# Optimization experiments

Measured on AMD Instinct MI355X. Metric: run time of the kernel, lower is better.

## Reference

```python
import jax, jax.numpy as jnp
import numpy as np

B, NAT, K, F, L = 16, 256, 24, 128, 4
EPS = 0.01  # action / displacement step scale


def _gather(a, idx):
    # a: [B, n, ...], idx: [B, n, k] -> [B, n, k, ...]
    return jax.vmap(lambda ab, ib: ab[ib])(a, idx)


def _knn_idx(x, cell, k):
    # periodic minimum-image kNN within each structure
    frac = x[:, None, :, :] - x[:, :, None, :]          # [B,i,j,3] = x_j - x_i
    frac = frac - jnp.round(frac)
    cart = jnp.einsum('bijd,bde->bije', frac, cell)
    dist = jnp.linalg.norm(cart, axis=-1)
    dist = dist + jnp.eye(x.shape[1], dtype=x.dtype) * 1e6  # exclude self
    _, idx = jax.lax.top_k(-dist, k)
    return idx


def _edge_vectors(x, cell, idx):
    xj = _gather(x, idx)                                # [B,n,k,3]
    frac = xj - x[:, :, None, :]
    frac = frac - jnp.round(frac)
    vec = jnp.einsum('bnkd,bde->bnke', frac, cell)
    dist = jnp.linalg.norm(vec, axis=-1)
    return vec, dist


def _mpnn(h, idx, dist, W1, b1, W2, b2):
    hj = _gather(h, idx)                                # [B,n,k,F]
    feat = jnp.concatenate([hj, dist[..., None]], axis=-1)
    m = jax.nn.silu(jnp.einsum('bnkf,fg->bnkg', feat, W1) + b1)
    return h + jax.nn.silu(m.sum(axis=2) @ W2 + b2)


def _forward(cell, x, z, emb, mW1, mb1, mW2, mb2, uW1, ub1, uW2, ub2, act_we, actpos_we):
    I = jnp.eye(3, dtype=x.dtype)
    Bc = cell.shape[0]
    cell0 = jnp.broadcast_to(I, (Bc, 3, 3))            # actions_init overrides input cell
    x = jnp.mod(x, 1.0)
    idx = _knn_idx(x, cell0, K)
    vec, dist = _edge_vectors(x, cell0, idx)
    u = vec / (dist[..., None] + 1e-12)
    cross = jnp.cross(u[:, :, :, None, :], u[:, :, None, :, :])  # [B,n,k,k,3]
    tri_mask = (jnp.linalg.norm(cross, axis=-1) > 1e-3).astype(x.dtype)  # filter_triplets

    h = emb[z]
    for l in range(L):
        h = _mpnn(h, idx, dist, mW1[l], mb1[l], mW2[l], mb2[l])

    action_rho = jnp.broadcast_to(I, (Bc, 3, 3))
    traj_sum = jnp.zeros_like(x)
    geo_cell = cell0
    rho_prime = action_rho
    for l in range(L):
        h = _mpnn(h, idx, dist, uW1[l], ub1[l], uW2[l], ub2[l])
        hj = _gather(h, idx)
        e_feat = h[:, :, None, :] + hj                  # [B,n,k,F]
        w_e = jnp.tanh(jnp.einsum('bnkf,f->bnk', e_feat, act_we[l]))
        w_t = w_e[:, :, :, None] * w_e[:, :, None, :] * tri_mask
        strain = jnp.einsum('bnk,bnkc,bnkd->bcd', w_e, u, u) / (NAT * K)
        tri = jnp.einsum('bnjk,bnjkc,bnjkd->bcd', w_t, cross, cross) / (NAT * K * K)
        action = jnp.eye(3, dtype=x.dtype) + EPS * (strain + tri)
        action_rho = jnp.einsum('bij,bjk->bik', action, action_rho)
        rho_prime = jnp.einsum('bij,bjk->bik', action_rho, cell0)
        # position actions
        w_p = jnp.tanh(jnp.einsum('bnkf,f->bnk', e_feat, actpos_we[l]))
        x_cart = EPS * jnp.einsum('bnk,bnkc->bnc', w_p, vec)
        x_frac = jnp.einsum('bnc,bcd->bnd', x_cart, jnp.linalg.inv(geo_cell))
        traj_sum = traj_sum + x_cart
        x = x + x_frac
        geo_cell = rho_prime
        vec, dist = _edge_vectors(x, geo_cell, idx)     # geometry.update_vectors()
        u = vec / (dist[..., None] + 1e-12)
        cross = jnp.cross(u[:, :, :, None, :], u[:, :, None, :, :])
    return traj_sum, rho_prime


def setup_inputs() -> dict:
    key = jax.random.key(0)
    ks = jax.random.split(key, 12)
    s1 = 1.0 / np.sqrt(F + 1)
    s2 = 1.0 / np.sqrt(F)
    return {
        'cell': jax.random.normal(ks[0], (B, 3, 3), jnp.float32),
        'x': jax.random.uniform(ks[1], (B, NAT, 3), jnp.float32),
        'z': jax.random.randint(ks[2], (B, NAT), 0, 100, dtype=jnp.int32),
        'struct_size': jnp.full((B,), NAT, dtype=jnp.int32),
        'emb': jax.random.normal(ks[3], (100, F), jnp.float32) * 0.1,
        'mpnn_W1': jax.random.normal(ks[4], (L, F + 1, F), jnp.float32) * s1,
        'mpnn_b1': jnp.zeros((L, F), jnp.float32),
        'mpnn_W2': jax.random.normal(ks[5], (L, F, F), jnp.float32) * s2,
        'mpnn_b2': jnp.zeros((L, F), jnp.float32),
        'upd_W1': jax.random.normal(ks[6], (L, F + 1, F), jnp.float32) * s1,
        'upd_b1': jnp.zeros((L, F), jnp.float32),
        'upd_W2': jax.random.normal(ks[7], (L, F, F), jnp.float32) * s2,
        'upd_b2': jnp.zeros((L, F), jnp.float32),
        'act_we': jax.random.normal(ks[8], (L, F), jnp.float32) * s2,
        'actpos_we': jax.random.normal(ks[9], (L, F), jnp.float32) * s2,
    }


def reference(cell, x, z, struct_size, emb, mpnn_W1, mpnn_b1, mpnn_W2, mpnn_b2, upd_W1, upd_b1, upd_W2, upd_b2, act_we, actpos_we):
    # struct_size is informational (dense uniform batch of NAT atoms per structure)
    return _forward(cell, x, z, emb, mpnn_W1, mpnn_b1, mpnn_W2, mpnn_b2,
                    upd_W1, upd_b1, upd_W2, upd_b2, act_we, actpos_we)
```

## Files before the change

kernel.cpp:

```cpp
#include <hip/hip_runtime.h>

#define NB 16
#define NATS 256
#define KNN 24
#define FD 128
#define EPSA 0.01f
#define NATOMS (NB * NATS)
#define NEDGE (NATOMS * KNN)

__device__ __forceinline__ float silu_f(float v) { return v / (1.f + __expf(-v)); }

__global__ __launch_bounds__(256) void init_gemm1_kernel(
    const float* __restrict__ xin, const int* __restrict__ z,
    const float* __restrict__ emb, const float* __restrict__ W1,
    float* __restrict__ x, float* __restrict__ traj,
    float* __restrict__ h, float* __restrict__ hW)
{
    __shared__ float As[128 * 18];
    __shared__ float Bs[128 * 128];
    const int t = threadIdx.x;
    const int atom0 = blockIdx.x * 16;
    if (t < 48) {
        int gi = atom0 * 3 + t;
        float v = xin[gi];
        x[gi] = v - floorf(v);
        traj[gi] = 0.f;
    }
    {
        const int r = t >> 4;
        const int f0 = (t & 15) * 8;
        const int a = atom0 + r;
        const float4* src = (const float4*)(emb + z[a] * FD + f0);
        float4 v0 = src[0], v1 = src[1];
        float4* dst = (float4*)(h + a * FD + f0);
        dst[0] = v0; dst[1] = v1;
        As[(f0 + 0) * 18 + r] = v0.x; As[(f0 + 1) * 18 + r] = v0.y;
        As[(f0 + 2) * 18 + r] = v0.z; As[(f0 + 3) * 18 + r] = v0.w;
        As[(f0 + 4) * 18 + r] = v1.x; As[(f0 + 5) * 18 + r] = v1.y;
        As[(f0 + 6) * 18 + r] = v1.z; As[(f0 + 7) * 18 + r] = v1.w;
    }
    {
        const float4* B4 = (const float4*)W1;
        float4* Bs4 = (float4*)Bs;
#pragma unroll
        for (int i = 0; i < 16; ++i) Bs4[t + i * 256] = B4[t + i * 256];
    }
    __syncthreads();
    const int ng = t & 31, mg = t >> 5;
    const int n0 = ng * 4, m0 = mg * 2;
    float a00 = 0, a01 = 0, a02 = 0, a03 = 0, a10 = 0, a11 = 0, a12 = 0, a13 = 0;
#pragma unroll 8
    for (int f = 0; f < 128; ++f) {
        float2 av = *(const float2*)&As[f * 18 + m0];
        float4 bv = *(const float4*)&Bs[f * FD + n0];
        a00 += av.x * bv.x; a01 += av.x * bv.y; a02 += av.x * bv.z; a03 += av.x * bv.w;
        a10 += av.y * bv.x; a11 += av.y * bv.y; a12 += av.y * bv.z; a13 += av.y * bv.w;
    }
    int row = atom0 + m0;
    *(float4*)(hW + row * FD + n0) = make_float4(a00, a01, a02, a03);
    *(float4*)(hW + (row + 1) * FD + n0) = make_float4(a10, a11, a12, a13);
}

__global__ __launch_bounds__(64) void knn_kernel(const float* __restrict__ x,
    int* __restrict__ idxb, float* __restrict__ u0, float* __restrict__ dist0)
{
    const int a = blockIdx.x;
    const int b = a >> 8;
    const int lane = threadIdx.x;
    const float xi0 = x[a * 3 + 0], xi1 = x[a * 3 + 1], xi2 = x[a * 3 + 2];
    unsigned long long key[4];
#pragma unroll
    for (int tt = 0; tt < 4; ++tt) {
        int jg = b * NATS + lane + tt * 64;
        float d0 = x[jg * 3 + 0] - xi0; d0 -= rintf(d0);
        float d1 = x[jg * 3 + 1] - xi1; d1 -= rintf(d1);
        float d2 = x[jg * 3 + 2] - xi2; d2 -= rintf(d2);
        float dd = sqrtf(d0 * d0 + d1 * d1 + d2 * d2);
        if (jg == a) dd += 1e6f;
        key[tt] = ((unsigned long long)__float_as_uint(dd) << 32) | (unsigned)jg;
    }
    int myj = 0;
    for (int sel = 0; sel < KNN; ++sel) {
        unsigned long long m = key[0];
        if (key[1] < m) m = key[1];
        if (key[2] < m) m = key[2];
        if (key[3] < m) m = key[3];
#pragma unroll
        for (int off = 32; off > 0; off >>= 1) {
            unsigned lo = (unsigned)__shfl_xor((int)(unsigned)(m & 0xffffffffu), off);
            unsigned hi = (unsigned)__shfl_xor((int)(unsigned)(m >> 32), off);
            unsigned long long o = ((unsigned long long)hi << 32) | lo;
            if (o < m) m = o;
        }
        int jw = (int)(m & 0xffffffffu);
        if (lane == 0) idxb[a * KNN + sel] = jw;
        if (lane == sel) myj = jw;
#pragma unroll
        for (int tt = 0; tt < 4; ++tt) if (key[tt] == m) key[tt] = ~0ull;
    }
    if (lane < KNN) {
        float f0 = x[myj * 3 + 0] - xi0; f0 -= rintf(f0);
        float f1 = x[myj * 3 + 1] - xi1; f1 -= rintf(f1);
        float f2 = x[myj * 3 + 2] - xi2; f2 -= rintf(f2);
        float dd = sqrtf(f0 * f0 + f1 * f1 + f2 * f2);
        float inv = 1.f / (dd + 1e-12f);
        int e = a * KNN + lane;
        u0[e * 3 + 0] = f0 * inv; u0[e * 3 + 1] = f1 * inv; u0[e * 3 + 2] = f2 * inv;
        dist0[e] = dd;
    }
}

__global__ __launch_bounds__(256, 2) void layer_kernel(
    const float* __restrict__ hW, const int* __restrict__ idxb,
    const float* __restrict__ dist0,
    const float* __restrict__ x, const float* __restrict__ geo, int use_geo,
    const float* __restrict__ wl, const float* __restrict__ b1,
    const float* __restrict__ W2, const float* __restrict__ b2,
    const float* __restrict__ W1n, float* __restrict__ hWout,
    float* __restrict__ h,
    const float* __restrict__ we_a, const float* __restrict__ we_p,
    float* __restrict__ p, float* __restrict__ q)
{
    __shared__ float As[128 * 9];
    __shared__ float sH[128 * 9];
    __shared__ float Bs[128 * 128];
    __shared__ int   sIdx[8 * KNN];
    __shared__ float sDist[8 * KNN];
    const int t = threadIdx.x;
    const int atom0 = blockIdx.x * 8;
    if (t < 8 * KNN) {
        int a = atom0 + (t / KNN);
        int j = idxb[atom0 * KNN + t];
        sIdx[t] = j;
        float d;
        if (dist0 != nullptr) {
            d = dist0[atom0 * KNN + t];
        } else {
            float f0 = x[j * 3 + 0] - x[a * 3 + 0]; f0 -= rintf(f0);
            float f1 = x[j * 3 + 1] - x[a * 3 + 1]; f1 -= rintf(f1);
            float f2 = x[j * 3 + 2] - x[a * 3 + 2]; f2 -= rintf(f2);
            float v0 = f0, v1 = f1, v2 = f2;
            if (use_geo) {
                const float* c = geo + (a >> 8) * 9;
                v0 = f0 * c[0] + f1 * c[3] + f2 * c[6];
                v1 = f0 * c[1] + f1 * c[4] + f2 * c[7];
                v2 = f0 * c[2] + f1 * c[5] + f2 * c[8];
            }
            d = sqrtf(v0 * v0 + v1 * v1 + v2 * v2);
        }
        sDist[t] = d;
    }
    __syncthreads();
    {
        const int g = t & 127;
        const int sub = t >> 7;
        const float wlg = wl[g];
        const float b1g = b1[g];
#pragma unroll
        for (int rep = 0; rep < 4; ++rep) {
            const int a = rep * 2 + sub;
            float s = 0.f;
#pragma unroll 8
            for (int k = 0; k < KNN; ++k) {
                int j = sIdx[a * KNN + k];
                float v = hW[j * FD + g] + sDist[a * KNN + k] * wlg + b1g;
                s += silu_f(v);
            }
            As[g * 9 + a] = s;
        }
    }
    {
        const float4* B4 = (const float4*)W2;
        float4* Bs4 = (float4*)Bs;
#pragma unroll
        for (int i = 0; i < 16; ++i) Bs4[t + i * 256] = B4[t + i * 256];
    }
    __syncthreads();
    const int ng = t & 31, mg = t >> 5;
    const int n0 = ng * 4;
    float c0 = 0, c1 = 0, c2 = 0, c3 = 0;
#pragma unroll 8
    for (int f = 0; f < 128; ++f) {
        float av = As[f * 9 + mg];
        float4 bv = *(const float4*)&Bs[f * FD + n0];
        c0 += av * bv.x; c1 += av * bv.y; c2 += av * bv.z; c3 += av * bv.w;
    }
    const int row = atom0 + mg;
    float4 bb = *(const float4*)(b2 + n0);
    float4 h0 = *(float4*)(h + row * FD + n0);
    float4 o0;
    o0.x = h0.x + silu_f(c0 + bb.x); o0.y = h0.y + silu_f(c1 + bb.y);
    o0.z = h0.z + silu_f(c2 + bb.z); o0.w = h0.w + silu_f(c3 + bb.w);
    *(float4*)(h + row * FD + n0) = o0;
    sH[(n0 + 0) * 9 + mg] = o0.x; sH[(n0 + 1) * 9 + mg] = o0.y;
    sH[(n0 + 2) * 9 + mg] = o0.z; sH[(n0 + 3) * 9 + mg] = o0.w;
    if (we_a != nullptr) {
        float4 wa = *(const float4*)(we_a + n0);
        float4 wp = *(const float4*)(we_p + n0);
        float p0 = o0.x * wa.x + o0.y * wa.y + o0.z * wa.z + o0.w * wa.w;
        float q0 = o0.x * wp.x + o0.y * wp.y + o0.z * wp.z + o0.w * wp.w;
#pragma unroll
        for (int off = 16; off > 0; off >>= 1) {
            p0 += __shfl_xor(p0, off); q0 += __shfl_xor(q0, off);
        }
        if (ng == 0) { p[row] = p0; q[row] = q0; }
    }
    if (W1n != nullptr) {
        __syncthreads();
        {
            const float4* B4 = (const float4*)W1n;
            float4* Bs4 = (float4*)Bs;
#pragma unroll
            for (int i = 0; i < 16; ++i) Bs4[t + i * 256] = B4[t + i * 256];
        }
        __syncthreads();
        float d0 = 0, d1 = 0, d2 = 0, d3 = 0;
#pragma unroll 8
        for (int f = 0; f < 128; ++f) {
            float av = sH[f * 9 + mg];
            float4 bv = *(const float4*)&Bs[f * FD + n0];
            d0 += av * bv.x; d1 += av * bv.y; d2 += av * bv.z; d3 += av * bv.w;
        }
        *(float4*)(hWout + row * FD + n0) = make_float4(d0, d1, d2, d3);
    }
}

__global__ __launch_bounds__(256) void accum_kernel(
    const float* __restrict__ p, const float* __restrict__ q,
    const int* __restrict__ idxb, const float* __restrict__ x,
    const float* __restrict__ geo, int use_geo,
    const float* __restrict__ u0b,
    float* __restrict__ part, float* __restrict__ xcart)
{
    const int blk = blockIdx.x;
    const int t = threadIdx.x;
    const int w = t >> 6;
    const int lane = t & 63;
    const int a = blk * 4 + w;
    const int b = a >> 8;
    __shared__ float swe[4][KNN], swp[4][KNN];
    __shared__ float su[4][KNN][3], su0[4][KNN][3], sv[4][KNN][3];
    __shared__ float spart[4][18];
    if (lane < KNN) {
        int e = a * KNN + lane;
        int j = idxb[e];
        swe[w][lane] = tanhf(p[a] + p[j]);
        swp[w][lane] = tanhf(q[a] + q[j]);
        float f0 = x[j * 3 + 0] - x[a * 3 + 0]; f0 -= rintf(f0);
        float f1 = x[j * 3 + 1] - x[a * 3 + 1]; f1 -= rintf(f1);
        float f2 = x[j * 3 + 2] - x[a * 3 + 2]; f2 -= rintf(f2);
        float v0 = f0, v1 = f1, v2 = f2;
        if (use_geo) {
            const float* c = geo + b * 9;
            v0 = f0 * c[0] + f1 * c[3] + f2 * c[6];
            v1 = f0 * c[1] + f1 * c[4] + f2 * c[7];
            v2 = f0 * c[2] + f1 * c[5] + f2 * c[8];
        }
        float dd = sqrtf(v0 * v0 + v1 * v1 + v2 * v2);
        float inv = 1.f / (dd + 1e-12f);
        sv[w][lane][0] = v0; sv[w][lane][1] = v1; sv[w][lane][2] = v2;
        su[w][lane][0] = v0 * inv; su[w][lane][1] = v1 * inv; su[w][lane][2] = v2 * inv;
        su0[w][lane][0] = u0b[e * 3]; su0[w][lane][1] = u0b[e * 3 + 1]; su0[w][lane][2] = u0b[e * 3 + 2];
    }
    __syncthreads();
    float r[21];
#pragma unroll
    for (int i = 0; i < 21; ++i) r[i] = 0.f;
    if (lane < KNN) {
        float wgt = swe[w][lane];
        float ux = su[w][lane][0], uy = su[w][lane][1], uz = su[w][lane][2];
        r[0] = wgt * ux * ux; r[1] = wgt * ux * uy; r[2] = wgt * ux * uz;
        r[3] = wgt * uy * ux; r[4] = wgt * uy * uy; r[5] = wgt * uy * uz;
        r[6] = wgt * uz * ux; r[7] = wgt * uz * uy; r[8] = wgt * uz * uz;
        float wp = swp[w][lane];
        r[18] = wp * sv[w][lane][0]; r[19] = wp * sv[w][lane][1]; r[20] = wp * sv[w][lane][2];
    }
#pragma unroll
    for (int tt = 0; tt < 9; ++tt) {
        int pr = lane + (tt << 6);
        int j = pr / KNN, k = pr - j * KNN;
        float c0x = su0[w][j][1] * su0[w][k][2] - su0[w][j][2] * su0[w][k][1];
        float c0y = su0[w][j][2] * su0[w][k][0] - su0[w][j][0] * su0[w][k][2];
        float c0z = su0[w][j][0] * su0[w][k][1] - su0[w][j][1] * su0[w][k][0];
        float nn2 = c0x * c0x + c0y * c0y + c0z * c0z;
        if (nn2 > 1e-6f) {
            float cx = su[w][j][1] * su[w][k][2] - su[w][j][2] * su[w][k][1];
            float cy = su[w][j][2] * su[w][k][0] - su[w][j][0] * su[w][k][2];
            float cz = su[w][j][0] * su[w][k][1] - su[w][j][1] * su[w][k][0];
            float wt = swe[w][j] * swe[w][k];
            r[9]  += wt * cx * cx; r[10] += wt * cx * cy; r[11] += wt * cx * cz;
            r[12] += wt * cy * cx; r[13] += wt * cy * cy; r[14] += wt * cy * cz;
            r[15] += wt * cz * cx; r[16] += wt * cz * cy; r[17] += wt * cz * cz;
        }
    }
#pragma unroll
    for (int off = 32; off > 0; off >>= 1)
#pragma unroll
        for (int i = 0; i < 21; ++i) r[i] += __shfl_down(r[i], off);
    if (lane == 0) {
#pragma unroll
        for (int i = 0; i < 18; ++i) spart[w][i] = r[i];
        xcart[a * 3 + 0] = EPSA * r[18];
        xcart[a * 3 + 1] = EPSA * r[19];
        xcart[a * 3 + 2] = EPSA * r[20];
    }
    __syncthreads();
    if (t < 18)
        part[blk * 18 + t] = spart[0][t] + spart[1][t] + spart[2][t] + spart[3][t];
}

__global__ __launch_bounds__(256) void rho_pos_kernel(const float* __restrict__ part,
    const float* __restrict__ xcart,
    float* __restrict__ rho, float* __restrict__ geo,
    float* __restrict__ x, float* __restrict__ traj,
    float* __restrict__ out, int first, int last)
{
    const int b = blockIdx.x;
    const int t = threadIdx.x;
    __shared__ float sIV[9];
    if (t < 64) {
        float r[18];
#pragma unroll
        for (int i = 0; i < 18; ++i) r[i] = part[(b * 64 + t) * 18 + i];
#pragma unroll
        for (int off = 32; off > 0; off >>= 1)
#pragma unroll
            for (int i = 0; i < 18; ++i) r[i] += __shfl_down(r[i], off);
        if (t == 0) {
            float A[9];
#pragma unroll
            for (int i = 0; i < 9; ++i) {
                float strain = r[i] / 6144.f;
                float tri = r[9 + i] / 147456.f;
                A[i] = ((i == 0 || i == 4 || i == 8) ? 1.f : 0.f) + EPSA * (strain + tri);
            }
            float N[9], IV[9];
            if (first) {
#pragma unroll
                for (int i = 0; i < 9; ++i) { N[i] = A[i]; IV[i] = (i == 0 || i == 4 || i == 8) ? 1.f : 0.f; }
            } else {
                float R[9], G[9];
#pragma unroll
                for (int i = 0; i < 9; ++i) { R[i] = rho[b * 9 + i]; G[i] = geo[b * 9 + i]; }
#pragma unroll
                for (int i = 0; i < 3; ++i)
#pragma unroll
                    for (int k = 0; k < 3; ++k)
                        N[i * 3 + k] = A[i * 3] * R[k] + A[i * 3 + 1] * R[3 + k] + A[i * 3 + 2] * R[6 + k];
                float det = G[0] * (G[4] * G[8] - G[5] * G[7])
                          - G[1] * (G[3] * G[8] - G[5] * G[6])
                          + G[2] * (G[3] * G[7] - G[4] * G[6]);
                float id = 1.f / det;
                IV[0] = (G[4] * G[8] - G[5] * G[7]) * id;
                IV[1] = (G[2] * G[7] - G[1] * G[8]) * id;
                IV[2] = (G[1] * G[5] - G[2] * G[4]) * id;
                IV[3] = (G[5] * G[6] - G[3] * G[8]) * id;
                IV[4] = (G[0] * G[8] - G[2] * G[6]) * id;
                IV[5] = (G[2] * G[3] - G[0] * G[5]) * id;
                IV[6] = (G[3] * G[7] - G[4] * G[6]) * id;
                IV[7] = (G[1] * G[6] - G[0] * G[7]) * id;
                IV[8] = (G[0] * G[4] - G[1] * G[3]) * id;
            }
#pragma unroll
            for (int i = 0; i < 9; ++i) {
                sIV[i] = IV[i];
                rho[b * 9 + i] = N[i];
                if (!last) geo[b * 9 + i] = N[i];
                else out[NATOMS * 3 + b * 9 + i] = N[i];
            }
        }
    }
    __syncthreads();
    for (int d = t; d < NATS * 3; d += 256) {
        int al = d / 3, dim = d - al * 3;
        int ga = b * NATS + al;
        int gi = ga * 3 + dim;
        float c0 = xcart[ga * 3 + 0], c1 = xcart[ga * 3 + 1], c2 = xcart[ga * 3 + 2];
        float tj = traj[gi] + xcart[gi];
        if (!last) {
            float xf = c0 * sIV[0 + dim] + c1 * sIV[3 + dim] + c2 * sIV[6 + dim];
            x[gi] += xf;
            traj[gi] = tj;
        } else {
            out[gi] = tj;
        }
    }
}

extern "C" void kernel_launch(void* const* d_in, const int* in_sizes, int n_in,
                              void* d_out, int out_size, void* d_ws, size_t ws_size,
                              hipStream_t stream)
{
    (void)in_sizes; (void)n_in; (void)out_size; (void)ws_size;
    const float* in_x = (const float*)d_in[1];
    const int*   z    = (const int*)d_in[2];
    const float* emb  = (const float*)d_in[4];
    const float* mW1  = (const float*)d_in[5];
    const float* mb1  = (const float*)d_in[6];
    const float* mW2  = (const float*)d_in[7];
    const float* mb2  = (const float*)d_in[8];
    const float* uW1  = (const float*)d_in[9];
    const float* ub1  = (const float*)d_in[10];
    const float* uW2  = (const float*)d_in[11];
    const float* ub2  = (const float*)d_in[12];
    const float* awe  = (const float*)d_in[13];
    const float* pwe  = (const float*)d_in[14];
    float* out = (float*)d_out;

    char* wsb = (char*)d_ws;
    size_t off = 0;
    auto carve = [&](size_t elems) {
        void* ptr = wsb + off;
        off += (elems * 4 + 255) & ~(size_t)255;
        return ptr;
    };
    float* traj  = (float*)carve(NATOMS * 3);
    float* part  = (float*)carve(1024 * 18);
    float* x     = (float*)carve(NATOMS * 3);
    float* xcart = (float*)carve(NATOMS * 3);
    float* p     = (float*)carve(NATOMS);
    float* q     = (float*)carve(NATOMS);
    float* rho   = (float*)carve(NB * 9);
    float* geo   = (float*)carve(NB * 9);
    float* u0    = (float*)carve(NEDGE * 3);
    float* dist0 = (float*)carve(NEDGE);
    float* h     = (float*)carve(NATOMS * FD);
    float* hWa   = (float*)carve(NATOMS * FD);
    float* hWb   = (float*)carve(NATOMS * FD);
    int*   idx   = (int*)carve(NEDGE);

    init_gemm1_kernel<<<256, 256, 0, stream>>>(in_x, z, emb, mW1, x, traj, h, hWa);
    knn_kernel<<<NATOMS, 64, 0, stream>>>(x, idx, u0, dist0);

    float* hw_in = hWa;
    float* hw_out = hWb;

    for (int l = 0; l < 4; ++l) {
        const float* W1n = (l < 3) ? (mW1 + (l + 1) * 129 * 128) : uW1;
        layer_kernel<<<512, 256, 0, stream>>>(hw_in, idx, dist0, x, geo, 0,
            mW1 + l * 129 * 128 + 128 * 128, mb1 + l * 128,
            mW2 + l * 128 * 128, mb2 + l * 128,
            W1n, hw_out, h,
            nullptr, nullptr, nullptr, nullptr);
        float* tmp = hw_in; hw_in = hw_out; hw_out = tmp;
    }
    for (int l = 0; l < 4; ++l) {
        const float* W1n = (l < 3) ? (uW1 + (l + 1) * 129 * 128) : nullptr;
        const float* d0 = (l == 0) ? dist0 : nullptr;
        layer_kernel<<<512, 256, 0, stream>>>(hw_in, idx, d0, x, geo, (l > 0) ? 1 : 0,
            uW1 + l * 129 * 128 + 128 * 128, ub1 + l * 128,
            uW2 + l * 128 * 128, ub2 + l * 128,
            W1n, hw_out, h,
            awe + l * 128, pwe + l * 128, p, q);
        float* tmp = hw_in; hw_in = hw_out; hw_out = tmp;
        accum_kernel<<<1024, 256, 0, stream>>>(p, q, idx, x, geo, (l > 0) ? 1 : 0,
            u0, part, xcart);
        rho_pos_kernel<<<NB, 256, 0, stream>>>(part, xcart, rho, geo, x, traj, out,
            (l == 0) ? 1 : 0, (l == 3) ? 1 : 0);
    }
}
```

Before: 347.5 us.

## Use split-bf16 MFMA for dense GEMMs with pre-transposed bf16 weight pairs

Adds a prep kernel that transposes every W1/W2 weight matrix and splits it into high and low bf16 halves. The init and layer GEMMs now run on 16x16x32 bf16 MFMA with three products per tile (hi*hi, hi*lo, lo*hi) to keep near-fp32 accuracy. The 64KB fp32 weight staging in LDS is removed in favour of direct global loads of B fragments, which also cuts LDS use per block. Only half of each 16-row MFMA tile holds real atoms in layer_kernel, so half the matrix work is wasted. The h write is also skipped on the last layer, and the geo transform is applied unconditionally.

```diff
diff --git a/kernel.cpp b/kernel.cpp
--- a/kernel.cpp
+++ b/kernel.cpp
@@ -8,16 +8,55 @@
 #define NATOMS (NB * NATS)
 #define NEDGE (NATOMS * KNN)
 
+typedef __attribute__((ext_vector_type(8))) short short8;
+typedef __attribute__((ext_vector_type(4))) float f32x4;
+
 __device__ __forceinline__ float silu_f(float v) { return v / (1.f + __expf(-v)); }
 
-__global__ __launch_bounds__(256) void init_gemm1_kernel(
+__device__ __forceinline__ short f2b(float f) {
+    union { float f; unsigned u; } v; v.f = f;
+    unsigned r = v.u + 0x7FFFu + ((v.u >> 16) & 1u);
+    return (short)(r >> 16);
+}
+__device__ __forceinline__ float b2f(short s) {
+    return __uint_as_float(((unsigned)(unsigned short)s) << 16);
+}
+__device__ __forceinline__ short8 ldb(const short* __restrict__ W, int n, int ks, int quad) {
+    return *(const short8*)&W[n * 128 + ks * 32 + quad * 8];
+}
+
+__global__ __launch_bounds__(256) void prep_kernel(
+    const float* __restrict__ mW1, const float* __restrict__ mW2,
+    const float* __restrict__ uW1, const float* __restrict__ uW2,
+    short* __restrict__ wh, short* __restrict__ wl_)
+{
+    int tid = blockIdx.x * 256 + threadIdx.x;
+    int m = tid >> 14;
+    int e = tid & 16383;
+    int n = e >> 7, k = e & 127;
+    const float* src;
+    int l = m & 3;
+    switch (m >> 2) {
+        case 0:  src = mW1 + l * 129 * 128; break;
+        case 1:  src = mW2 + l * 128 * 128; break;
+        case 2:  src = uW1 + l * 129 * 128; break;
+        default: src = uW2 + l * 128 * 128; break;
+    }
+    float w = src[k * 128 + n];
+    short hi = f2b(w);
+    wh[tid] = hi;
+    wl_[tid] = f2b(w - b2f(hi));
+}
+
+__global__ __launch_bounds__(256) void init_kernel(
     const float* __restrict__ xin, const int* __restrict__ z,
-    const float* __restrict__ emb, const float* __restrict__ W1,
+    const float* __restrict__ emb,
+    const short* __restrict__ W1h, const short* __restrict__ W1l,
     float* __restrict__ x, float* __restrict__ traj,
     float* __restrict__ h, float* __restrict__ hW)
 {
-    __shared__ float As[128 * 18];
-    __shared__ float Bs[128 * 128];
+    __shared__ short sAH[16 * 136];
+    __shared__ short sAL[16 * 136];
     const int t = threadIdx.x;
     const int atom0 = blockIdx.x * 16;
     if (t < 48) {
@@ -34,31 +73,45 @@
         float4 v0 = src[0], v1 = src[1];
         float4* dst = (float4*)(h + a * FD + f0);
         dst[0] = v0; dst[1] = v1;
-        As[(f0 + 0) * 18 + r] = v0.x; As[(f0 + 1) * 18 + r] = v0.y;
-        As[(f0 + 2) * 18 + r] = v0.z; As[(f0 + 3) * 18 + r] = v0.w;
-        As[(f0 + 4) * 18 + r] = v1.x; As[(f0 + 5) * 18 + r] = v1.y;
-        As[(f0 + 6) * 18 + r] = v1.z; As[(f0 + 7) * 18 + r] = v1.w;
-    }
-    {
-        const float4* B4 = (const float4*)W1;
-        float4* Bs4 = (float4*)Bs;
-#pragma unroll
-        for (int i = 0; i < 16; ++i) Bs4[t + i * 256] = B4[t + i * 256];
-    }
-    __syncthreads();
-    const int ng = t & 31, mg = t >> 5;
-    const int n0 = ng * 4, m0 = mg * 2;
-    float a00 = 0, a01 = 0, a02 = 0, a03 = 0, a10 = 0, a11 = 0, a12 = 0, a13 = 0;
-#pragma unroll 8
-    for (int f = 0; f < 128; ++f) {
-        float2 av = *(const float2*)&As[f * 18 + m0];
-        float4 bv = *(const float4*)&Bs[f * FD + n0];
-        a00 += av.x * bv.x; a01 += av.x * bv.y; a02 += av.x * bv.z; a03 += av.x * bv.w;
-        a10 += av.y * bv.x; a11 += av.y * bv.y; a12 += av.y * bv.z; a13 += av.y * bv.w;
-    }
-    int row = atom0 + m0;
-    *(float4*)(hW + row * FD + n0) = make_float4(a00, a01, a02, a03);
-    *(float4*)(hW + (row + 1) * FD + n0) = make_float4(a10, a11, a12, a13);
+        float vv[8] = {v0.x, v0.y, v0.z, v0.w, v1.x, v1.y, v1.z, v1.w};
+        short8 shv, slv;
+#pragma unroll
+        for (int i = 0; i < 8; ++i) {
+            short hi = f2b(vv[i]);
+            shv[i] = hi; slv[i] = f2b(vv[i] - b2f(hi));
+        }
+        *(short8*)&sAH[r * 136 + f0] = shv;
+        *(short8*)&sAL[r * 136 + f0] = slv;
+    }
+    __syncthreads();
+    const int w = t >> 6, lane = t & 63, quad = lane >> 4, col = lane & 15;
+    const int n0 = w * 32;
+    f32x4 acc0 = {0.f, 0.f, 0.f, 0.f}, acc1 = {0.f, 0.f, 0.f, 0.f};
+#pragma unroll
+    for (int ks = 0; ks < 4; ++ks) {
+        short8 ah = *(const short8*)&sAH[col * 136 + ks * 32 + quad * 8];
+        short8 al = *(const short8*)&sAL[col * 136 + ks * 32 + quad * 8];
+        short8 bh0 = ldb(W1h, n0 + col, ks, quad);
+        short8 bl0 = ldb(W1l, n0 + col, ks, quad);
+        short8 bh1 = ldb(W1h, n0 + 16 + col, ks, quad);
+        short8 bl1 = ldb(W1l, n0 + 16 + col, ks, quad);
+        acc0 = __builtin_amdgcn_mfma_f32_16x16x32_bf16(ah, bh0, acc0, 0, 0, 0);
+        acc0 = __builtin_amdgcn_mfma_f32_16x16x32_bf16(ah, bl0, acc0, 0, 0, 0);
+        acc0 = __builtin_amdgcn_mfma_f32_16x16x32_bf16(al, bh0, acc0, 0, 0, 0);
+        acc1 = __builtin_amdgcn_mfma_f32_16x16x32_bf16(ah, bh1, acc1, 0, 0, 0);
+        acc1 = __builtin_amdgcn_mfma_f32_16x16x32_bf16(ah, bl1, acc1, 0, 0, 0);
+        acc1 = __builtin_amdgcn_mfma_f32_16x16x32_bf16(al, bh1, acc1, 0, 0, 0);
+    }
+#pragma unroll
+    for (int nt = 0; nt < 2; ++nt) {
+        int gn = n0 + nt * 16 + col;
+        f32x4 av = (nt == 0) ? acc0 : acc1;
+#pragma unroll
+        for (int r = 0; r < 4; ++r) {
+            int row = quad * 4 + r;
+            hW[(atom0 + row) * FD + gn] = av[r];
+        }
+    }
 }
 
 __global__ __launch_bounds__(64) void knn_kernel(const float* __restrict__ x,
@@ -115,15 +168,19 @@
     const float* __restrict__ dist0,
     const float* __restrict__ x, const float* __restrict__ geo, int use_geo,
     const float* __restrict__ wl, const float* __restrict__ b1,
-    const float* __restrict__ W2, const float* __restrict__ b2,
-    const float* __restrict__ W1n, float* __restrict__ hWout,
-    float* __restrict__ h,
+    const short* __restrict__ W2h, const short* __restrict__ W2l,
+    const float* __restrict__ b2,
+    const short* __restrict__ W1nh, const short* __restrict__ W1nl,
+    float* __restrict__ hWout,
+    float* __restrict__ h, int write_h,
     const float* __restrict__ we_a, const float* __restrict__ we_p,
     float* __restrict__ p, float* __restrict__ q)
 {
-    __shared__ float As[128 * 9];
-    __shared__ float sH[128 * 9];
-    __shared__ float Bs[128 * 128];
+    __shared__ short sAggH[16 * 136];
+    __shared__ short sAggL[16 * 136];
+    __shared__ short sHnH[16 * 136];
+    __shared__ short sHnL[16 * 136];
+    __shared__ float sHf[8 * 136];
     __shared__ int   sIdx[8 * KNN];
     __shared__ float sDist[8 * KNN];
     const int t = threadIdx.x;
@@ -139,13 +196,10 @@
             float f0 = x[j * 3 + 0] - x[a * 3 + 0]; f0 -= rintf(f0);
             float f1 = x[j * 3 + 1] - x[a * 3 + 1]; f1 -= rintf(f1);
             float f2 = x[j * 3 + 2] - x[a * 3 + 2]; f2 -= rintf(f2);
-            float v0 = f0, v1 = f1, v2 = f2;
-            if (use_geo) {
-                const float* c = geo + (a >> 8) * 9;
-                v0 = f0 * c[0] + f1 * c[3] + f2 * c[6];
-                v1 = f0 * c[1] + f1 * c[4] + f2 * c[7];
-                v2 = f0 * c[2] + f1 * c[5] + f2 * c[8];
-            }
+            const float* c = geo + (a >> 8) * 9;
+            float v0 = f0 * c[0] + f1 * c[3] + f2 * c[6];
+            float v1 = f0 * c[1] + f1 * c[4] + f2 * c[7];
+            float v2 = f0 * c[2] + f1 * c[5] + f2 * c[8];
             d = sqrtf(v0 * v0 + v1 * v1 + v2 * v2);
         }
         sDist[t] = d;
@@ -166,62 +220,94 @@
                 float v = hW[j * FD + g] + sDist[a * KNN + k] * wlg + b1g;
                 s += silu_f(v);
             }
-            As[g * 9 + a] = s;
-        }
-    }
-    {
-        const float4* B4 = (const float4*)W2;
-        float4* Bs4 = (float4*)Bs;
-#pragma unroll
-        for (int i = 0; i < 16; ++i) Bs4[t + i * 256] = B4[t + i * 256];
-    }
-    __syncthreads();
-    const int ng = t & 31, mg = t >> 5;
-    const int n0 = ng * 4;
-    float c0 = 0, c1 = 0, c2 = 0, c3 = 0;
-#pragma unroll 8
-    for (int f = 0; f < 128; ++f) {
-        float av = As[f * 9 + mg];
-        float4 bv = *(const float4*)&Bs[f * FD + n0];
-        c0 += av * bv.x; c1 += av * bv.y; c2 += av * bv.z; c3 += av * bv.w;
-    }
-    const int row = atom0 + mg;
-    float4 bb = *(const float4*)(b2 + n0);
-    float4 h0 = *(float4*)(h + row * FD + n0);
-    float4 o0;
-    o0.x = h0.x + silu_f(c0 + bb.x); o0.y = h0.y + silu_f(c1 + bb.y);
-    o0.z = h0.z + silu_f(c2 + bb.z); o0.w = h0.w + silu_f(c3 + bb.w);
-    *(float4*)(h + row * FD + n0) = o0;
-    sH[(n0 + 0) * 9 + mg] = o0.x; sH[(n0 + 1) * 9 + mg] = o0.y;
-    sH[(n0 + 2) * 9 + mg] = o0.z; sH[(n0 + 3) * 9 + mg] = o0.w;
-    if (we_a != nullptr) {
-        float4 wa = *(const float4*)(we_a + n0);
-        float4 wp = *(const float4*)(we_p + n0);
-        float p0 = o0.x * wa.x + o0.y * wa.y + o0.z * wa.z + o0.w * wa.w;
-        float q0 = o0.x * wp.x + o0.y * wp.y + o0.z * wp.z + o0.w * wp.w;
-#pragma unroll
-        for (int off = 16; off > 0; off >>= 1) {
-            p0 += __shfl_xor(p0, off); q0 += __shfl_xor(q0, off);
-        }
-        if (ng == 0) { p[row] = p0; q[row] = q0; }
-    }
-    if (W1n != nullptr) {
-        __syncthreads();
-        {
-            const float4* B4 = (const float4*)W1n;
-            float4* Bs4 = (float4*)Bs;
-#pragma unroll
-            for (int i = 0; i < 16; ++i) Bs4[t + i * 256] = B4[t + i * 256];
-        }
-        __syncthreads();
-        float d0 = 0, d1 = 0, d2 = 0, d3 = 0;
-#pragma unroll 8
-        for (int f = 0; f < 128; ++f) {
-            float av = sH[f * 9 + mg];
-            float4 bv = *(const float4*)&Bs[f * FD + n0];
-            d0 += av * bv.x; d1 += av * bv.y; d2 += av * bv.z; d3 += av * bv.w;
-        }
-        *(float4*)(hWout + row * FD + n0) = make_float4(d0, d1, d2, d3);
+            short hi = f2b(s);
+            sAggH[a * 136 + g] = hi;
+            sAggL[a * 136 + g] = f2b(s - b2f(hi));
+        }
+    }
+    __syncthreads();
+    const int w = t >> 6, lane = t & 63, quad = lane >> 4, col = lane & 15;
+    const int n0 = w * 32;
+    f32x4 acc0 = {0.f, 0.f, 0.f, 0.f}, acc1 = {0.f, 0.f, 0.f, 0.f};
+#pragma unroll
+    for (int ks = 0; ks < 4; ++ks) {
+        short8 ah = *(const short8*)&sAggH[col * 136 + ks * 32 + quad * 8];
+        short8 al = *(const short8*)&sAggL[col * 136 + ks * 32 + quad * 8];
+        short8 bh0 = ldb(W2h, n0 + col, ks, quad);
+        short8 bl0 = ldb(W2l, n0 + col, ks, quad);
+        short8 bh1 = ldb(W2h, n0 + 16 + col, ks, quad);
+        short8 bl1 = ldb(W2l, n0 + 16 + col, ks, quad);
+        acc0 = __builtin_amdgcn_mfma_f32_16x16x32_bf16(ah, bh0, acc0, 0, 0, 0);
+        acc0 = __builtin_amdgcn_mfma_f32_16x16x32_bf16(ah, bl0, acc0, 0, 0, 0);
+        acc0 = __builtin_amdgcn_mfma_f32_16x16x32_bf16(al, bh0, acc0, 0, 0, 0);
+        acc1 = __builtin_amdgcn_mfma_f32_16x16x32_bf16(ah, bh1, acc1, 0, 0, 0);
+        acc1 = __builtin_amdgcn_mfma_f32_16x16x32_bf16(ah, bl1, acc1, 0, 0, 0);
+        acc1 = __builtin_amdgcn_mfma_f32_16x16x32_bf16(al, bh1, acc1, 0, 0, 0);
+    }
+#pragma unroll
+    for (int nt = 0; nt < 2; ++nt) {
+        int gn = n0 + nt * 16 + col;
+        float bb = b2[gn];
+        f32x4 av = (nt == 0) ? acc0 : acc1;
+#pragma unroll
+        for (int r = 0; r < 4; ++r) {
+            int row = quad * 4 + r;
+            if (row < 8) {
+                float o = h[(atom0 + row) * FD + gn] + silu_f(av[r] + bb);
+                if (write_h) h[(atom0 + row) * FD + gn] = o;
+                short hi = f2b(o);
+                sHnH[row * 136 + gn] = hi;
+                sHnL[row * 136 + gn] = f2b(o - b2f(hi));
+                sHf[row * 136 + gn] = o;
+            }
+        }
+    }
+    __syncthreads();
+    if (we_a != nullptr && t < 128) {
+        int a = t >> 4, gr = t & 15;
+        float pp = 0.f, qq = 0.f;
+#pragma unroll
+        for (int i = 0; i < 8; ++i) {
+            int g = gr + i * 16;
+            float hv = sHf[a * 136 + g];
+            pp += hv * we_a[g];
+            qq += hv * we_p[g];
+        }
+#pragma unroll
+        for (int off = 8; off >= 1; off >>= 1) {
+            pp += __shfl_xor(pp, off);
+            qq += __shfl_xor(qq, off);
+        }
+        if (gr == 0) { p[atom0 + a] = pp; q[atom0 + a] = qq; }
+    }
+    if (W1nh != nullptr) {
+        f32x4 d0 = {0.f, 0.f, 0.f, 0.f}, d1 = {0.f, 0.f, 0.f, 0.f};
+#pragma unroll
+        for (int ks = 0; ks < 4; ++ks) {
+            short8 ah = *(const short8*)&sHnH[col * 136 + ks * 32 + quad * 8];
+            short8 al = *(const short8*)&sHnL[col * 136 + ks * 32 + quad * 8];
+            short8 bh0 = ldb(W1nh, n0 + col, ks, quad);
+            short8 bl0 = ldb(W1nl, n0 + col, ks, quad);
+            short8 bh1 = ldb(W1nh, n0 + 16 + col, ks, quad);
+            short8 bl1 = ldb(W1nl, n0 + 16 + col, ks, quad);
+            d0 = __builtin_amdgcn_mfma_f32_16x16x32_bf16(ah, bh0, d0, 0, 0, 0);
+            d0 = __builtin_amdgcn_mfma_f32_16x16x32_bf16(ah, bl0, d0, 0, 0, 0);
+            d0 = __builtin_amdgcn_mfma_f32_16x16x32_bf16(al, bh0, d0, 0, 0, 0);
+            d1 = __builtin_amdgcn_mfma_f32_16x16x32_bf16(ah, bh1, d1, 0, 0, 0);
+            d1 = __builtin_amdgcn_mfma_f32_16x16x32_bf16(ah, bl1, d1, 0, 0, 0);
+            d1 = __builtin_amdgcn_mfma_f32_16x16x32_bf16(al, bh1, d1, 0, 0, 0);
+        }
+#pragma unroll
+        for (int nt = 0; nt < 2; ++nt) {
+            int gn = n0 + nt * 16 + col;
+            f32x4 av = (nt == 0) ? d0 : d1;
+#pragma unroll
+            for (int r = 0; r < 4; ++r) {
+                int row = quad * 4 + r;
+                if (row < 8)
+                    hWout[(atom0 + row) * FD + gn] = av[r];
+            }
+        }
     }
 }
 
@@ -428,29 +514,36 @@
     float* hWa   = (float*)carve(NATOMS * FD);
     float* hWb   = (float*)carve(NATOMS * FD);
     int*   idx   = (int*)carve(NEDGE);
-
-    init_gemm1_kernel<<<256, 256, 0, stream>>>(in_x, z, emb, mW1, x, traj, h, hWa);
+    short* wth   = (short*)carve(16 * 16384 / 2);
+    short* wtl   = (short*)carve(16 * 16384 / 2);
+
+    auto WH = [&](int m) { return wth + m * 16384; };
+    auto WL = [&](int m) { return wtl + m * 16384; };
+
+    prep_kernel<<<1024, 256, 0, stream>>>(mW1, mW2, uW1, uW2, wth, wtl);
+    init_kernel<<<256, 256, 0, stream>>>(in_x, z, emb, WH(0), WL(0), x, traj, h, hWa);
     knn_kernel<<<NATOMS, 64, 0, stream>>>(x, idx, u0, dist0);
 
     float* hw_in = hWa;
     float* hw_out = hWb;
 
     for (int l = 0; l < 4; ++l) {
-        const float* W1n = (l < 3) ? (mW1 + (l + 1) * 129 * 128) : uW1;
+        int w1n = (l < 3) ? (l + 1) : 8;
         layer_kernel<<<512, 256, 0, stream>>>(hw_in, idx, dist0, x, geo, 0,
             mW1 + l * 129 * 128 + 128 * 128, mb1 + l * 128,
-            mW2 + l * 128 * 128, mb2 + l * 128,
-            W1n, hw_out, h,
+            WH(4 + l), WL(4 + l), mb2 + l * 128,
+            WH(w1n), WL(w1n), hw_out, h, 1,
             nullptr, nullptr, nullptr, nullptr);
         float* tmp = hw_in; hw_in = hw_out; hw_out = tmp;
     }
     for (int l = 0; l < 4; ++l) {
-        const float* W1n = (l < 3) ? (uW1 + (l + 1) * 129 * 128) : nullptr;
+        const short* W1nh = (l < 3) ? WH(9 + l) : nullptr;
+        const short* W1nl = (l < 3) ? WL(9 + l) : nullptr;
         const float* d0 = (l == 0) ? dist0 : nullptr;
         layer_kernel<<<512, 256, 0, stream>>>(hw_in, idx, d0, x, geo, (l > 0) ? 1 : 0,
             uW1 + l * 129 * 128 + 128 * 128, ub1 + l * 128,
-            uW2 + l * 128 * 128, ub2 + l * 128,
-            W1n, hw_out, h,
+            WH(12 + l), WL(12 + l), ub2 + l * 128,
+            W1nh, W1nl, hw_out, h, (l < 3) ? 1 : 0,
             awe + l * 128, pwe + l * 128, p, q);
         float* tmp = hw_in; hw_in = hw_out; hw_out = tmp;
         accum_kernel<<<1024, 256, 0, stream>>>(p, q, idx, x, geo, (l > 0) ? 1 : 0,
```

After: 339.1 us. 1.02x faster.
